# Optimization experiments

Hardware: AMD Instinct MI355X
Metric: run time of the kernel (lower is better)

## Reference

```python
import jax, jax.numpy as jnp
import numpy as np

NUM_EXPERTS = 8
TOP_K = 2
HIDDEN = 2048
INTER = 7168
NUM_TOKENS = 8192


def setup_inputs() -> dict:
    key = jax.random.key(0)
    k0, k1, k2, k3, k4 = jax.random.split(key, 5)
    hidden_states = jax.random.normal(k0, (NUM_TOKENS, HIDDEN), dtype=jnp.float32)
    gate_w = jax.random.normal(k1, (NUM_EXPERTS, HIDDEN), dtype=jnp.float32) / 10.0
    w1 = jax.random.normal(k2, (NUM_EXPERTS, INTER, HIDDEN), dtype=jnp.float32) / 10.0
    w3 = jax.random.normal(k3, (NUM_EXPERTS, INTER, HIDDEN), dtype=jnp.float32) / 10.0
    w2 = jax.random.normal(k4, (NUM_EXPERTS, HIDDEN, INTER), dtype=jnp.float32) / 10.0
    return {"hidden_states": hidden_states, "gate_w": gate_w, "w1": w1, "w3": w3, "w2": w2}


def reference(hidden_states, gate_w, w1, w3, w2):
    x = hidden_states  # [T, H]
    num_experts = gate_w.shape[0]
    # router
    router_logits = x @ gate_w.T  # [T, E]
    probs = jax.nn.softmax(router_logits.astype(jnp.float32), axis=-1)
    top_w, top_i = jax.lax.top_k(probs, TOP_K)              # [T, K]
    top_w = top_w / jnp.sum(top_w, axis=-1, keepdims=True)  # renormalize
    top_w = top_w.astype(x.dtype)
    # dense [T, E] routing weight (0 for unselected experts)
    expert_ids = jnp.arange(num_experts)
    w_dense = jnp.sum(
        jnp.where(top_i[:, :, None] == expert_ids[None, None, :], top_w[:, :, None], 0.0),
        axis=1,
    )  # [T, E]
    out = jnp.zeros_like(x)
    for e in range(num_experts):
        g = jax.nn.silu(x @ w1[e].T) * (x @ w3[e].T)  # [T, I]
        out = out + w_dense[:, e:e + 1] * (g @ w2[e].T)
    return out
```

## Files before the change

kernel.cpp:

```cpp
#include <hip/hip_runtime.h>

#define NTOK 8192
#define HID 2048
#define ITR 7168
#define NE 8
#define BK32 32
#define TILE32 (128 * BK32)

typedef __attribute__((ext_vector_type(8))) short short8;
typedef __attribute__((ext_vector_type(8))) __bf16 bf16x8;
typedef __attribute__((ext_vector_type(4))) float f32x4;

__device__ __forceinline__ unsigned short f2bf(float f) {
  unsigned int u = __float_as_uint(f);
  u += 0x7FFFu + ((u >> 16) & 1u);
  return (unsigned short)(u >> 16);
}

__device__ __forceinline__ f32x4 mfma_bf16(short8 a, short8 b, f32x4 c) {
  union U { short8 s; bf16x8 b; };
  U ua; ua.s = a;
  U ub; ub.s = b;
  return __builtin_amdgcn_mfma_f32_16x16x32_bf16(ua.b, ub.b, c, 0, 0, 0);
}

typedef __attribute__((address_space(1))) const unsigned int g_u32;
typedef __attribute__((address_space(3))) unsigned int l_u32;

__device__ __forceinline__ void gload16(const unsigned short* src, unsigned short* dst) {
  __builtin_amdgcn_global_load_lds((g_u32*)src, (l_u32*)dst, 16, 0, 0);
}

__device__ __forceinline__ short8 read_frag32(const unsigned short* base, int row, int kelem) {
  int slot = ((row << 2) + (kelem >> 3)) ^ (row & 7);
  return *reinterpret_cast<const short8*>(reinterpret_cast<const char*>(base) + slot * 16);
}

__device__ __forceinline__ void slot_src(int s, int* row, int* c) {
  int r0 = ((s >> 2) ^ (s >> 4)) & 1;
  *row = ((s >> 2) & ~1) | r0;
  *c = ((s ^ r0) & 1) | ((((s >> 1) ^ (s >> 3)) & 1) << 1);
}

#define VMCNT(N) asm volatile("s_waitcnt vmcnt(" #N ")" ::: "memory")
#define BARRIER()                         \
  do {                                    \
    __builtin_amdgcn_s_barrier();         \
    asm volatile("" ::: "memory");        \
  } while (0)

__global__ __launch_bounds__(256) void moe_router(
    const float* __restrict__ x, const float* __restrict__ gw,
    int* __restrict__ cnt, int* __restrict__ pair_token, float* __restrict__ pair_w,
    int4* __restrict__ tok_ep) {
  int wave = threadIdx.x >> 6;
  int lane = threadIdx.x & 63;
  int t = blockIdx.x * 4 + wave;
  const float4* xr = reinterpret_cast<const float4*>(x + (size_t)t * HID);
  float acc[NE];
#pragma unroll
  for (int e = 0; e < NE; ++e) acc[e] = 0.f;
#pragma unroll
  for (int j = 0; j < 8; ++j) {
    int c = lane + 64 * j;
    float4 xv = xr[c];
#pragma unroll
    for (int e = 0; e < NE; ++e) {
      float4 gv = reinterpret_cast<const float4*>(gw + (size_t)e * HID)[c];
      acc[e] += xv.x * gv.x + xv.y * gv.y + xv.z * gv.z + xv.w * gv.w;
    }
  }
#pragma unroll
  for (int e = 0; e < NE; ++e) {
    float s = acc[e];
#pragma unroll
    for (int m = 32; m > 0; m >>= 1) s += __shfl_xor(s, m);
    acc[e] = s;
  }
  if (lane == 0) {
    int e0 = 0; float l0 = acc[0];
#pragma unroll
    for (int e = 1; e < NE; ++e) if (acc[e] > l0) { l0 = acc[e]; e0 = e; }
    int e1 = -1; float l1 = -3.0e38f;
#pragma unroll
    for (int e = 0; e < NE; ++e) if (e != e0 && acc[e] > l1) { l1 = acc[e]; e1 = e; }
    float z = __expf(l1 - l0);
    float w0 = 1.f / (1.f + z);
    float w1 = z / (1.f + z);
    int p0 = atomicAdd(&cnt[e0], 1);
    pair_token[e0 * NTOK + p0] = t;
    pair_w[e0 * NTOK + p0] = w0;
    int p1 = atomicAdd(&cnt[e1], 1);
    pair_token[e1 * NTOK + p1] = t;
    pair_w[e1 * NTOK + p1] = w1;
    tok_ep[t] = make_int4(e0, e1, p0, p1);
  }
}

__global__ void moe_scan(const int* __restrict__ cnt, int* __restrict__ base) {
  if (threadIdx.x == 0) {
    int s = 0;
#pragma unroll
    for (int e = 0; e < NE; ++e) { base[e] = s; s += cnt[e]; }
  }
}

__global__ __launch_bounds__(256) void moe_cvt(const float* __restrict__ src,
                                               unsigned short* __restrict__ dst) {
  size_t i = (size_t)blockIdx.x * 256 + threadIdx.x;
  const float4* p = reinterpret_cast<const float4*>(src) + i * 2;
  float4 a = p[0], b = p[1];
  union { unsigned short us[8]; short8 v; } u;
  u.us[0] = f2bf(a.x); u.us[1] = f2bf(a.y); u.us[2] = f2bf(a.z); u.us[3] = f2bf(a.w);
  u.us[4] = f2bf(b.x); u.us[5] = f2bf(b.y); u.us[6] = f2bf(b.z); u.us[7] = f2bf(b.w);
  reinterpret_cast<short8*>(dst)[i] = u.v;
}


__global__ __launch_bounds__(256, 2) void moe_gemm1_e(
    const unsigned short* __restrict__ xb, const unsigned short* __restrict__ w1b,
    const unsigned short* __restrict__ w3b, const int* __restrict__ cnt,
    const int* __restrict__ base, const int* __restrict__ pair_token,
    unsigned short* __restrict__ g) {
  int e = blockIdx.z;
  int n_e = cnt[e];
  int rowTile = blockIdx.x;
  if (rowTile * 128 >= n_e) return;
  int colTile = blockIdx.y;

  __shared__ unsigned short lds[3 * 3 * TILE32];

  int tid = threadIdx.x;
  int lane = tid & 63;
  int wv = tid >> 6;
  int wr = wv >> 1, wc = wv & 1;
  int lr = lane & 15;
  int lk = (lane >> 4) * 8;

  int slotP = e * NTOK + rowTile * 128;
  int slotG = base[e] + rowTile * 128;
  const unsigned short* w1e = w1b + (size_t)e * ITR * HID + (size_t)colTile * 128 * HID;
  const unsigned short* w3e = w3b + (size_t)e * ITR * HID + (size_t)colTile * 128 * HID;

  const unsigned short* a_s[2];
  const unsigned short* b1_s[2];
  const unsigned short* b3_s[2];
#pragma unroll
  for (int i = 0; i < 2; ++i) {
    int s = wv * 128 + i * 64 + lane;
    int row, c;
    slot_src(s, &row, &c);
    int tok = pair_token[slotP + ((rowTile * 128 + row < n_e) ? row : 0)];
    a_s[i] = xb + (size_t)tok * HID + c * 8;
    b1_s[i] = w1e + (size_t)row * HID + c * 8;
    b3_s[i] = w3e + (size_t)row * HID + c * 8;
  }

  f32x4 acc1[4][4], acc3[4][4];
#pragma unroll
  for (int m = 0; m < 4; ++m)
#pragma unroll
    for (int n = 0; n < 4; ++n) {
      acc1[m][n] = (f32x4){0.f, 0.f, 0.f, 0.f};
      acc3[m][n] = (f32x4){0.f, 0.f, 0.f, 0.f};
    }

#define STAGE1(buf, koff)                                                        \
  do {                                                                           \
    unsigned short* Lb = lds + (buf) * 3 * TILE32 + wv * 1024;                   \
    _Pragma("unroll") for (int i = 0; i < 2; ++i) {                              \
      gload16(a_s[i] + (koff), Lb + i * 512);                                    \
      gload16(b1_s[i] + (koff), Lb + TILE32 + i * 512);                          \
      gload16(b3_s[i] + (koff), Lb + 2 * TILE32 + i * 512);                      \
    }                                                                            \
  } while (0)

  const int nt = HID / BK32;
  STAGE1(0, 0);
  STAGE1(1, BK32);

  for (int t = 0; t < nt; ++t) {
    if (t + 1 < nt) VMCNT(6); else VMCNT(0);
    BARRIER();

    const unsigned short* A = lds + (t % 3) * 3 * TILE32;
    const unsigned short* B1 = A + TILE32;
    const unsigned short* B3 = A + 2 * TILE32;
    short8 av[4];
#pragma unroll
    for (int m = 0; m < 4; ++m) av[m] = read_frag32(A, wr * 64 + m * 16 + lr, lk);
#pragma unroll
    for (int n = 0; n < 4; ++n) {
      short8 b1v = read_frag32(B1, wc * 64 + n * 16 + lr, lk);
      short8 b3v = read_frag32(B3, wc * 64 + n * 16 + lr, lk);
#pragma unroll
      for (int m = 0; m < 4; ++m) {
        acc1[m][n] = mfma_bf16(av[m], b1v, acc1[m][n]);
        acc3[m][n] = mfma_bf16(av[m], b3v, acc3[m][n]);
      }
    }

    if (t + 2 < nt) STAGE1((t + 2) % 3, (t + 2) * BK32);
  }
#undef STAGE1

#pragma unroll
  for (int m = 0; m < 4; ++m) {
    int rbase = wr * 64 + m * 16 + ((lane >> 4) << 2);
#pragma unroll
    for (int r = 0; r < 4; ++r) {
      int rt = rbase + r;
      if (rowTile * 128 + rt < n_e) {
        unsigned short* grow = g + (size_t)(slotG + rt) * ITR + colTile * 128 + wc * 64;
#pragma unroll
        for (int n = 0; n < 4; ++n) {
          float h1 = acc1[m][n][r], h3 = acc3[m][n][r];
          float sl = h1 / (1.f + __expf(-h1));
          grow[n * 16 + lr] = f2bf(sl * h3);
        }
      }
    }
  }
}

#define G2H_BUF 12288

__global__ __launch_bounds__(256, 2) void moe_gemm2_h(
    const unsigned short* __restrict__ g, const unsigned short* __restrict__ w2b,
    const int* __restrict__ cnt, const int* __restrict__ base,
    const float* __restrict__ pair_w, float* __restrict__ part) {
  int e = blockIdx.z;
  int n_e = cnt[e];
  int rowTile = blockIdx.x;
  if (rowTile * 256 >= n_e) return;
  int colTile = blockIdx.y;

  __shared__ unsigned short lds[3 * G2H_BUF];

  int tid = threadIdx.x;
  int lane = tid & 63;
  int wv = tid >> 6;
  int wr = wv >> 1;
  int wc = wv & 1;
  int lr = lane & 15;
  int lk = (lane >> 4) * 8;

  int slotP = e * NTOK + rowTile * 256;
  int slotG = base[e] + rowTile * 256;
  const unsigned short* w2e = w2b + (size_t)e * HID * ITR + (size_t)colTile * 128 * ITR;

  const unsigned short* a_s[4];
  const unsigned short* b_s[2];
#pragma unroll
  for (int i = 0; i < 4; ++i) {
    int s = wv * 256 + i * 64 + lane;
    int row, c;
    slot_src(s, &row, &c);
    int rclamp = (rowTile * 256 + row < n_e) ? row : 0;
    a_s[i] = g + (size_t)(slotG + rclamp) * ITR + c * 8;
  }
#pragma unroll
  for (int i = 0; i < 2; ++i) {
    int s = wv * 128 + i * 64 + lane;
    int row, c;
    slot_src(s, &row, &c);
    b_s[i] = w2e + (size_t)row * ITR + c * 8;
  }

  f32x4 acc[8][4];
#pragma unroll
  for (int m = 0; m < 8; ++m)
#pragma unroll
    for (int n = 0; n < 4; ++n) acc[m][n] = (f32x4){0.f, 0.f, 0.f, 0.f};

#define STAGE2(buf, koff)                                                        \
  do {                                                                           \
    unsigned short* Lb = lds + (buf) * G2H_BUF;                                  \
    _Pragma("unroll") for (int i = 0; i < 4; ++i)                                \
      gload16(a_s[i] + (koff), Lb + wv * 2048 + i * 512);                        \
    _Pragma("unroll") for (int i = 0; i < 2; ++i)                                \
      gload16(b_s[i] + (koff), Lb + 8192 + wv * 1024 + i * 512);                 \
  } while (0)

  const int nt = ITR / BK32;
  STAGE2(0, 0);
  STAGE2(1, BK32);

  for (int t = 0; t < nt; ++t) {
    if (t + 1 < nt) VMCNT(6); else VMCNT(0);
    BARRIER();

    const unsigned short* A = lds + (t % 3) * G2H_BUF;
    const unsigned short* B = A + 8192;
    short8 av[8];
#pragma unroll
    for (int m = 0; m < 8; ++m) av[m] = read_frag32(A, wr * 128 + m * 16 + lr, lk);
#pragma unroll
    for (int n = 0; n < 4; ++n) {
      short8 bv = read_frag32(B, wc * 64 + n * 16 + lr, lk);
#pragma unroll
      for (int m = 0; m < 8; ++m) acc[m][n] = mfma_bf16(av[m], bv, acc[m][n]);
    }

    if (t + 2 < nt) STAGE2((t + 2) % 3, (t + 2) * BK32);
  }
#undef STAGE2

#pragma unroll
  for (int m = 0; m < 8; ++m) {
    int rbase = wr * 128 + m * 16 + ((lane >> 4) << 2);
#pragma unroll
    for (int r = 0; r < 4; ++r) {
      int rt = rbase + r;
      if (rowTile * 256 + rt < n_e) {
        float wgt = pair_w[slotP + rt];
        float* prow = part + (size_t)(slotG + rt) * HID + colTile * 128 + wc * 64;
#pragma unroll
        for (int n = 0; n < 4; ++n) prow[n * 16 + lr] = wgt * acc[m][n][r];
      }
    }
  }
}

__global__ __launch_bounds__(256) void moe_combine(
    const float* __restrict__ part, const int4* __restrict__ tok_ep,
    const int* __restrict__ base, float* __restrict__ out) {
  int t = blockIdx.x;
  int4 ep = tok_ep[t];
  int s0 = base[ep.x] + ep.z;
  int s1 = base[ep.y] + ep.w;
  const float4* p0 = reinterpret_cast<const float4*>(part + (size_t)s0 * HID);
  const float4* p1 = reinterpret_cast<const float4*>(part + (size_t)s1 * HID);
  float4* o = reinterpret_cast<float4*>(out + (size_t)t * HID);
#pragma unroll
  for (int i = 0; i < 2; ++i) {
    int idx = threadIdx.x + i * 256;
    float4 a = p0[idx], b = p1[idx];
    o[idx] = make_float4(a.x + b.x, a.y + b.y, a.z + b.z, a.w + b.w);
  }
}


extern "C" void kernel_launch(void* const* d_in, const int* in_sizes, int n_in,
                              void* d_out, int out_size, void* d_ws, size_t ws_size,
                              hipStream_t stream) {
  const float* x = (const float*)d_in[0];
  const float* gate_w = (const float*)d_in[1];
  const float* w1 = (const float*)d_in[2];
  const float* w3 = (const float*)d_in[3];
  const float* w2 = (const float*)d_in[4];
  float* out = (float*)d_out;

  char* ws = (char*)d_ws;
  const size_t WEL = (size_t)NE * ITR * HID;
  const size_t G_BYTES = (size_t)NTOK * 2 * ITR * 2;
  const size_t XB_BYTES = (size_t)NTOK * HID * 2;
  const size_t PAIR_BYTES = (size_t)NE * NTOK * 4;
  const size_t TOKEP_BYTES = (size_t)NTOK * 16;
  const size_t WB_BYTES = WEL * 2;

  unsigned short* g = (unsigned short*)ws;
  unsigned short* xb = (unsigned short*)(ws + G_BYTES);
  int* pair_token = (int*)(ws + G_BYTES + XB_BYTES);
  float* pair_w = (float*)(ws + G_BYTES + XB_BYTES + PAIR_BYTES);
  int4* tok_ep = (int4*)(ws + G_BYTES + XB_BYTES + 2 * PAIR_BYTES);
  int* cnt = (int*)(ws + G_BYTES + XB_BYTES + 2 * PAIR_BYTES + TOKEP_BYTES);
  int* base = cnt + NE;
  char* wbase = ws + G_BYTES + XB_BYTES + 2 * PAIR_BYTES + TOKEP_BYTES + 256;
  unsigned short* w1b = (unsigned short*)wbase;
  unsigned short* w3b = (unsigned short*)(wbase + WB_BYTES);
  unsigned short* w2b = (unsigned short*)(wbase + 2 * WB_BYTES);
  float* part = (float*)wbase;

  hipMemsetAsync(cnt, 0, 2 * NE * sizeof(int), stream);

  moe_router<<<NTOK / 4, 256, 0, stream>>>(x, gate_w, cnt, pair_token, pair_w, tok_ep);
  moe_scan<<<1, 64, 0, stream>>>(cnt, base);
  moe_cvt<<<(NTOK * HID) / 2048, 256, 0, stream>>>(x, xb);

  const int WGRID = (int)(WEL / 2048);
  moe_cvt<<<WGRID, 256, 0, stream>>>(w1, w1b);
  moe_cvt<<<WGRID, 256, 0, stream>>>(w3, w3b);
  moe_cvt<<<WGRID, 256, 0, stream>>>(w2, w2b);

  moe_gemm1_e<<<dim3(NTOK / 128, ITR / 128, NE), 256, 0, stream>>>(
      xb, w1b, w3b, cnt, base, pair_token, g);
  moe_gemm2_h<<<dim3(NTOK / 256, HID / 128, NE), 256, 0, stream>>>(
      g, w2b, cnt, base, pair_w, part);
  moe_combine<<<NTOK, 256, 0, stream>>>(part, tok_ep, base, out);
}
```

Before: 3.921 ms.

## Rewrite second expert GEMM as 256x256 tile, 8-wave ping-pong pipeline

Replaces the 256-thread, 256x128-tile down-projection GEMM with a 512-thread kernel computing 256x256 tiles. The K step grows to 64, split into two halves with double-buffered LDS. Global loads for the next step are interleaved between four MFMA sub-phases, and s_setprio raises priority around the MFMA clusters. The aim is more reuse of each loaded tile and better overlap of memory traffic with matrix math. The cost is more barriers per K step, a larger LDS footprint (128KB per block), and possibly lower occupancy.

After: 3.696 ms. 1.06x faster.

```diff
diff --git a/kernel.cpp b/kernel.cpp
--- a/kernel.cpp
+++ b/kernel.cpp
@@ -6,6 +6,8 @@
 #define NE 8
 #define BK32 32
 #define TILE32 (128 * BK32)
+#define G2P_HALF 8192
+#define G2P_BUF 32768
 
 typedef __attribute__((ext_vector_type(8))) short short8;
 typedef __attribute__((ext_vector_type(8))) __bf16 bf16x8;
@@ -116,7 +118,6 @@
   reinterpret_cast<short8*>(dst)[i] = u.v;
 }
 
-
 __global__ __launch_bounds__(256, 2) void moe_gemm1_e(
     const unsigned short* __restrict__ xb, const unsigned short* __restrict__ w1b,
     const unsigned short* __restrict__ w3b, const int* __restrict__ cnt,
@@ -223,9 +224,7 @@
   }
 }
 
-#define G2H_BUF 12288
-
-__global__ __launch_bounds__(256, 2) void moe_gemm2_h(
+__global__ __launch_bounds__(512, 2) void moe_gemm2_p(
     const unsigned short* __restrict__ g, const unsigned short* __restrict__ w2b,
     const int* __restrict__ cnt, const int* __restrict__ base,
     const float* __restrict__ pair_w, float* __restrict__ part) {
@@ -235,36 +234,30 @@
   if (rowTile * 256 >= n_e) return;
   int colTile = blockIdx.y;
 
-  __shared__ unsigned short lds[3 * G2H_BUF];
+  __shared__ unsigned short lds[2 * G2P_BUF];
 
   int tid = threadIdx.x;
   int lane = tid & 63;
   int wv = tid >> 6;
-  int wr = wv >> 1;
-  int wc = wv & 1;
+  int wr = wv >> 2;
+  int wc = wv & 3;
   int lr = lane & 15;
   int lk = (lane >> 4) * 8;
 
   int slotP = e * NTOK + rowTile * 256;
   int slotG = base[e] + rowTile * 256;
-  const unsigned short* w2e = w2b + (size_t)e * HID * ITR + (size_t)colTile * 128 * ITR;
-
-  const unsigned short* a_s[4];
-  const unsigned short* b_s[2];
-#pragma unroll
-  for (int i = 0; i < 4; ++i) {
-    int s = wv * 256 + i * 64 + lane;
+  const unsigned short* w2e = w2b + (size_t)e * HID * ITR + (size_t)colTile * 256 * ITR;
+
+  const unsigned short* aA[2];
+  const unsigned short* aB[2];
+#pragma unroll
+  for (int j = 0; j < 2; ++j) {
+    int s = j * 512 + tid;
     int row, c;
     slot_src(s, &row, &c);
     int rclamp = (rowTile * 256 + row < n_e) ? row : 0;
-    a_s[i] = g + (size_t)(slotG + rclamp) * ITR + c * 8;
-  }
-#pragma unroll
-  for (int i = 0; i < 2; ++i) {
-    int s = wv * 128 + i * 64 + lane;
-    int row, c;
-    slot_src(s, &row, &c);
-    b_s[i] = w2e + (size_t)row * ITR + c * 8;
+    aA[j] = g + (size_t)(slotG + rclamp) * ITR + c * 8;
+    aB[j] = w2e + (size_t)row * ITR + c * 8;
   }
 
   f32x4 acc[8][4];
@@ -273,38 +266,82 @@
 #pragma unroll
     for (int n = 0; n < 4; ++n) acc[m][n] = (f32x4){0.f, 0.f, 0.f, 0.f};
 
-#define STAGE2(buf, koff)                                                        \
+#define STG_A(buf, t_, h_)                                                       \
   do {                                                                           \
-    unsigned short* Lb = lds + (buf) * G2H_BUF;                                  \
-    _Pragma("unroll") for (int i = 0; i < 4; ++i)                                \
-      gload16(a_s[i] + (koff), Lb + wv * 2048 + i * 512);                        \
-    _Pragma("unroll") for (int i = 0; i < 2; ++i)                                \
-      gload16(b_s[i] + (koff), Lb + 8192 + wv * 1024 + i * 512);                 \
+    unsigned short* Lb = lds + (buf) * G2P_BUF + (h_) * G2P_HALF;                \
+    gload16(aA[0] + ((t_) * 64 + (h_) * 32), Lb + (wv * 64) * 8);                \
+    gload16(aA[1] + ((t_) * 64 + (h_) * 32), Lb + ((512 + wv * 64) * 8));        \
   } while (0)
-
-  const int nt = ITR / BK32;
-  STAGE2(0, 0);
-  STAGE2(1, BK32);
+#define STG_B(buf, t_, h_)                                                       \
+  do {                                                                           \
+    unsigned short* Lb = lds + (buf) * G2P_BUF + 16384 + (h_) * G2P_HALF;        \
+    gload16(aB[0] + ((t_) * 64 + (h_) * 32), Lb + (wv * 64) * 8);                \
+    gload16(aB[1] + ((t_) * 64 + (h_) * 32), Lb + ((512 + wv * 64) * 8));        \
+  } while (0)
+
+  const int nt = ITR / 64;
+  STG_A(0, 0, 0); STG_B(0, 0, 0); STG_A(0, 0, 1); STG_B(0, 0, 1);
+  VMCNT(4);
+  BARRIER();
 
   for (int t = 0; t < nt; ++t) {
-    if (t + 1 < nt) VMCNT(6); else VMCNT(0);
+    int cb = t & 1, nb = cb ^ 1;
+    const unsigned short* A0 = lds + cb * G2P_BUF;
+    const unsigned short* A1 = A0 + G2P_HALF;
+    const unsigned short* B0 = A0 + 2 * G2P_HALF;
+    const unsigned short* B1 = A0 + 3 * G2P_HALF;
+    short8 av[4], bv[4];
+
+#pragma unroll
+    for (int m = 0; m < 4; ++m) av[m] = read_frag32(A0, wr * 128 + m * 16 + lr, lk);
+#pragma unroll
+    for (int n = 0; n < 4; ++n) bv[n] = read_frag32(B0, wc * 64 + n * 16 + lr, lk);
+    if (t + 1 < nt) STG_A(nb, t + 1, 0);
     BARRIER();
-
-    const unsigned short* A = lds + (t % 3) * G2H_BUF;
-    const unsigned short* B = A + 8192;
-    short8 av[8];
-#pragma unroll
-    for (int m = 0; m < 8; ++m) av[m] = read_frag32(A, wr * 128 + m * 16 + lr, lk);
-#pragma unroll
-    for (int n = 0; n < 4; ++n) {
-      short8 bv = read_frag32(B, wc * 64 + n * 16 + lr, lk);
-#pragma unroll
-      for (int m = 0; m < 8; ++m) acc[m][n] = mfma_bf16(av[m], bv, acc[m][n]);
-    }
-
-    if (t + 2 < nt) STAGE2((t + 2) % 3, (t + 2) * BK32);
-  }
-#undef STAGE2
+    __builtin_amdgcn_s_setprio(1);
+#pragma unroll
+    for (int n = 0; n < 4; ++n)
+#pragma unroll
+      for (int m = 0; m < 4; ++m) acc[m][n] = mfma_bf16(av[m], bv[n], acc[m][n]);
+    __builtin_amdgcn_s_setprio(0);
+
+#pragma unroll
+    for (int m = 0; m < 4; ++m) av[m] = read_frag32(A0, wr * 128 + (m + 4) * 16 + lr, lk);
+    if (t + 1 < nt) { STG_B(nb, t + 1, 0); VMCNT(4); } else { VMCNT(0); }
+    BARRIER();
+    __builtin_amdgcn_s_setprio(1);
+#pragma unroll
+    for (int n = 0; n < 4; ++n)
+#pragma unroll
+      for (int m = 0; m < 4; ++m) acc[m + 4][n] = mfma_bf16(av[m], bv[n], acc[m + 4][n]);
+    __builtin_amdgcn_s_setprio(0);
+
+#pragma unroll
+    for (int m = 0; m < 4; ++m) av[m] = read_frag32(A1, wr * 128 + m * 16 + lr, lk);
+#pragma unroll
+    for (int n = 0; n < 4; ++n) bv[n] = read_frag32(B1, wc * 64 + n * 16 + lr, lk);
+    if (t + 1 < nt) STG_A(nb, t + 1, 1);
+    BARRIER();
+    __builtin_amdgcn_s_setprio(1);
+#pragma unroll
+    for (int n = 0; n < 4; ++n)
+#pragma unroll
+      for (int m = 0; m < 4; ++m) acc[m][n] = mfma_bf16(av[m], bv[n], acc[m][n]);
+    __builtin_amdgcn_s_setprio(0);
+
+#pragma unroll
+    for (int m = 0; m < 4; ++m) av[m] = read_frag32(A1, wr * 128 + (m + 4) * 16 + lr, lk);
+    if (t + 1 < nt) { STG_B(nb, t + 1, 1); VMCNT(4); }
+    BARRIER();
+    __builtin_amdgcn_s_setprio(1);
+#pragma unroll
+    for (int n = 0; n < 4; ++n)
+#pragma unroll
+      for (int m = 0; m < 4; ++m) acc[m + 4][n] = mfma_bf16(av[m], bv[n], acc[m + 4][n]);
+    __builtin_amdgcn_s_setprio(0);
+  }
+#undef STG_A
+#undef STG_B
 
 #pragma unroll
   for (int m = 0; m < 8; ++m) {
@@ -314,7 +351,7 @@
       int rt = rbase + r;
       if (rowTile * 256 + rt < n_e) {
         float wgt = pair_w[slotP + rt];
-        float* prow = part + (size_t)(slotG + rt) * HID + colTile * 128 + wc * 64;
+        float* prow = part + (size_t)(slotG + rt) * HID + colTile * 256 + wc * 64;
 #pragma unroll
         for (int n = 0; n < 4; ++n) prow[n * 16 + lr] = wgt * acc[m][n][r];
       }
@@ -385,7 +422,7 @@
 
   moe_gemm1_e<<<dim3(NTOK / 128, ITR / 128, NE), 256, 0, stream>>>(
       xb, w1b, w3b, cnt, base, pair_token, g);
-  moe_gemm2_h<<<dim3(NTOK / 256, HID / 128, NE), 256, 0, stream>>>(
+  moe_gemm2_p<<<dim3(NTOK / 256, HID / 256, NE), 512, 0, stream>>>(
       g, w2b, cnt, base, pair_w, part);
   moe_combine<<<NTOK, 256, 0, stream>>>(part, tok_ep, base, out);
 }
```
